# Kernel tuning notes

Hardware: AMD Instinct MI355X
Metric: run time of the kernel (lower is better)

The kernel has to match this reference:

```python
import jax, jax.numpy as jnp
import numpy as np

N_NODES = 100000
N_EDGES = 1600000
IN_DIM = 128
HIDDEN = 128
OUT_DIM = 10
N_GRAPHS = 512
N_LAYERS = 3


def setup_inputs() -> dict:
    key = jax.random.key(0)
    ks = jax.random.split(key, 12)
    s_in = 1.0 / np.sqrt(IN_DIM)
    s_h = 1.0 / np.sqrt(HIDDEN)
    return {
        "x": jax.random.normal(ks[0], (N_NODES, IN_DIM), jnp.float32),
        "lin1_w": jax.random.normal(ks[1], (IN_DIM, HIDDEN), jnp.float32) * s_in,
        "lin1_b": jnp.zeros((HIDDEN,), jnp.float32),
        "gcn_w": jax.random.normal(ks[2], (N_LAYERS, HIDDEN, HIDDEN), jnp.float32) * s_h,
        "gcn_b": jnp.zeros((N_LAYERS, HIDDEN), jnp.float32),
        "lin_out_w": jax.random.normal(ks[3], (HIDDEN, HIDDEN), jnp.float32) * s_h,
        "lin_out_b": jnp.zeros((HIDDEN,), jnp.float32),
        "cls_w": jax.random.normal(ks[4], (HIDDEN, OUT_DIM), jnp.float32) * s_h,
        "cls_b": jnp.zeros((OUT_DIM,), jnp.float32),
        "edge_index": jax.random.randint(ks[5], (2, N_EDGES), 0, N_NODES, jnp.int64),
        "batch": jnp.sort(jax.random.randint(ks[6], (N_NODES,), 0, N_GRAPHS, jnp.int64)),
    }


def reference(x, lin1_w, lin1_b, gcn_w, gcn_b, lin_out_w, lin_out_b, cls_w, cls_b, edge_index, batch):
    n = x.shape[0]
    # GCNConv normalization with added self-loops (PyG default)
    row, col = edge_index[0], edge_index[1]
    loop = jnp.arange(n)
    row2 = jnp.concatenate([row, loop])  # source (message origin)
    col2 = jnp.concatenate([col, loop])  # target (aggregation index)
    deg = jax.ops.segment_sum(jnp.ones_like(col2, dtype=x.dtype), col2, num_segments=n)
    dinv = jax.lax.rsqrt(jnp.maximum(deg, 1.0))
    norm = (dinv[row2] * dinv[col2])[:, None]  # [E+N, 1]

    counts = jax.ops.segment_sum(jnp.ones((n,), x.dtype), batch, num_segments=N_GRAPHS)
    counts = jnp.maximum(counts, 1.0)[:, None]

    def readout_mean(h):  # global_mean_pool -> [G, H]
        return jax.ops.segment_sum(h, batch, num_segments=N_GRAPHS) / counts

    # lin1 + elu (dropout = identity in eval mode)
    h = jax.nn.elu(x @ lin1_w + lin1_b)
    reps = readout_mean(h)  # readout_layers[0]; l_sum accumulates layer reps
    for i in range(N_LAYERS):
        hw = h @ gcn_w[i]                       # [N, H]
        msg = norm * hw[row2]                   # gather + scale
        agg = jax.ops.segment_sum(msg, col2, num_segments=n)  # scatter-add
        h = jax.nn.elu(agg + gcn_b[i])          # GCNConv bias then NaOp act
        # pooling op is 'none' (remove_pooling=True): graph unchanged
        reps = reps + readout_mean(h)           # readout_layers[i+1], summed by LaOp 'l_sum'
    g = jax.nn.elu(reps @ lin_out_w + lin_out_b)
    logits = g @ cls_w + cls_b
    return jax.nn.log_softmax(logits, axis=-1)
```

## Files before the change

### kernel.cpp

```cpp
#include <hip/hip_runtime.h>
#include <hip/hip_bf16.h>
#include <math.h>

#define NN 100000
#define NE 1600000
#define HID 128
#define NG 512
#define NB 512
#define RB 196
#define PCHUNK 4096
#define NPARTB ((NE + PCHUNK - 1) / PCHUNK)
#define GEMM_GRID ((NN + 127) / 128)

typedef unsigned short ushort_t;
typedef __attribute__((ext_vector_type(8))) short bf16x8;
typedef __attribute__((ext_vector_type(8))) unsigned short ushort8_t;
typedef __attribute__((ext_vector_type(4))) float f32x4;

__device__ __forceinline__ ushort_t f2bf(float v) {
    unsigned u = __float_as_uint(v);
    unsigned r = (u + 0x7FFF + ((u >> 16) & 1)) >> 16;
    return (ushort_t)r;
}
__device__ __forceinline__ float bf2f(ushort_t u) {
    return __uint_as_float((unsigned)u << 16);
}


__global__ __launch_bounds__(256) void hist_prepw(const int* __restrict__ ecol, int* __restrict__ bcount,
                                                  const float* __restrict__ lin1_w,
                                                  const float* __restrict__ gcn_w,
                                                  ushort_t* __restrict__ wt_hi,
                                                  ushort_t* __restrict__ wt_lo) {
    if (blockIdx.x < NPARTB) {
        __shared__ int lh[NB];
        const int blk = blockIdx.x, t = threadIdx.x;
        for (int i = t; i < NB; i += 256) lh[i] = 0;
        __syncthreads();
        const int e0 = blk * PCHUNK;
        const int e1 = min(e0 + PCHUNK, NE);
        for (int e = e0 + t; e < e1; e += 256) atomicAdd(&lh[ecol[e] / RB], 1);
        __syncthreads();
        for (int i = t; i < NB; i += 256) bcount[blk * NB + i] = lh[i];
    } else {
        int mb = blockIdx.x - NPARTB;
        int m = mb >> 3;
        int chunk = mb & 7;
        const float* W = (m == 0) ? lin1_w : gcn_w + (size_t)(m - 1) * 16384;
        ushort_t* hi = wt_hi + (size_t)m * 16384;
        ushort_t* lo = wt_lo + (size_t)m * 16384;
        for (int i = chunk * 2048 + threadIdx.x; i < (chunk + 1) * 2048; i += 256) {
            int j = i & 7;
            int lane = (i >> 3) & 63;
            int ks = (i >> 9) & 3;
            int ct = (i >> 11) & 7;
            int n = ct * 16 + (lane & 15);
            int k = ks * 32 + (lane >> 4) * 8 + j;
            float v = W[k * 128 + n];
            ushort_t h = f2bf(v);
            hi[i] = h;
            lo[i] = f2bf(v - bf2f(h));
        }
    }
}

__global__ __launch_bounds__(NB) void scan_bases(const int* __restrict__ bcount, int* __restrict__ basew,
                                                 int* __restrict__ brp, int* __restrict__ rp,
                                                 const int* __restrict__ batch, float* __restrict__ invcnt,
                                                 float* __restrict__ reps) {
    __shared__ int s[NB];
    int t = threadIdx.x;
    int tot = 0;
    for (int k = 0; k < NPARTB; ++k) {
        int c = bcount[k * NB + t];
        basew[k * NB + t] = tot;
        tot += c;
    }
    s[t] = tot;
    __syncthreads();
    for (int off = 1; off < NB; off <<= 1) {
        int x = (t >= off) ? s[t - off] : 0;
        __syncthreads();
        s[t] += x;
        __syncthreads();
    }
    int ex = s[t] - tot;
    brp[t] = ex;
    if (t == NB - 1) { brp[NB] = s[t]; rp[NN] = s[t]; }

    int lo = 0, hi = NN;
    while (lo < hi) { int m = (lo + hi) >> 1; if (batch[m] < t) lo = m + 1; else hi = m; }
    int s0 = lo;
    lo = 0; hi = NN;
    while (lo < hi) { int m = (lo + hi) >> 1; if (batch[m] < t + 1) lo = m + 1; else hi = m; }
    int c = lo - s0;
    invcnt[t] = 1.0f / (float)(c > 0 ? c : 1);

    f32x4 z = {0.f, 0.f, 0.f, 0.f};
    f32x4* rr = (f32x4*)(reps + (size_t)t * 128);
#pragma unroll
    for (int j = 0; j < 32; ++j) rr[j] = z;
}

template<int AMODE, int MODE>
__device__ __forceinline__ void gemm_body(int bid, int tid,
                                          const float* __restrict__ Af32,
                                          const ushort_t* __restrict__ a_bf,
                                          const ushort_t* __restrict__ wt_hi,
                                          const ushort_t* __restrict__ wt_lo,
                                          const float* __restrict__ bias,
                                          const float* __restrict__ dinv,
                                          ushort_t* __restrict__ out0,
                                          int N,
                                          ushort_t (* __restrict__ lt)[130]) {
    const int lane = tid & 63;
    const int wid = tid >> 6;
    const int rowBase = bid * 128 + wid * 32;
    const int rblk = rowBase >> 4;
    const int l15 = lane & 15, lg = lane >> 4;

    f32x4 acc[2][8];
#pragma unroll
    for (int rt = 0; rt < 2; ++rt)
#pragma unroll
        for (int ct = 0; ct < 8; ++ct) acc[rt][ct] = (f32x4){0.f, 0.f, 0.f, 0.f};

#pragma unroll
    for (int ks = 0; ks < 4; ++ks) {
        bf16x8 ahi[2], alo[2];
#pragma unroll
        for (int rt = 0; rt < 2; ++rt) {
            int r = rowBase + rt * 16 + l15;
            if (AMODE == 1) {
                float av[8];
                if (r < N) {
                    const float* ap = Af32 + (size_t)r * 128 + ks * 32 + lg * 8;
                    float4 a0 = *(const float4*)(ap);
                    float4 a1 = *(const float4*)(ap + 4);
                    av[0] = a0.x; av[1] = a0.y; av[2] = a0.z; av[3] = a0.w;
                    av[4] = a1.x; av[5] = a1.y; av[6] = a1.z; av[7] = a1.w;
                } else {
#pragma unroll
                    for (int j = 0; j < 8; ++j) av[j] = 0.f;
                }
#pragma unroll
                for (int j = 0; j < 8; ++j) {
                    ushort_t h = f2bf(av[j]);
                    ahi[rt][j] = (short)h;
                    alo[rt][j] = (short)f2bf(av[j] - bf2f(h));
                }
            } else {
                if (r < N) {
                    ahi[rt] = *(const bf16x8*)(a_bf + (size_t)(rblk + rt) * 2048 + (ks * 4 + lg) * 128 + l15 * 8);
                } else {
                    bf16x8 z = {0, 0, 0, 0, 0, 0, 0, 0};
                    ahi[rt] = z;
                }
            }
        }
#pragma unroll
        for (int ct = 0; ct < 8; ++ct) {
            size_t boff = (size_t)(((ct * 4 + ks) * 64 + lane) * 8);
            bf16x8 bhi = *(const bf16x8*)(wt_hi + boff);
            bf16x8 blo = *(const bf16x8*)(wt_lo + boff);
            acc[0][ct] = __builtin_amdgcn_mfma_f32_16x16x32_bf16(ahi[0], bhi, acc[0][ct], 0, 0, 0);
            acc[1][ct] = __builtin_amdgcn_mfma_f32_16x16x32_bf16(ahi[1], bhi, acc[1][ct], 0, 0, 0);
            acc[0][ct] = __builtin_amdgcn_mfma_f32_16x16x32_bf16(ahi[0], blo, acc[0][ct], 0, 0, 0);
            acc[1][ct] = __builtin_amdgcn_mfma_f32_16x16x32_bf16(ahi[1], blo, acc[1][ct], 0, 0, 0);
            if (AMODE == 1) {
                acc[0][ct] = __builtin_amdgcn_mfma_f32_16x16x32_bf16(alo[0], bhi, acc[0][ct], 0, 0, 0);
                acc[1][ct] = __builtin_amdgcn_mfma_f32_16x16x32_bf16(alo[1], bhi, acc[1][ct], 0, 0, 0);
            }
        }
    }

    if (MODE == 0) {
#pragma unroll
        for (int rt = 0; rt < 2; ++rt) {
#pragma unroll
            for (int reg = 0; reg < 4; ++reg) {
                int row = rowBase + rt * 16 + lg * 4 + reg;
                if (row >= N) continue;
                int r16 = lg * 4 + reg;
#pragma unroll
                for (int ct = 0; ct < 8; ++ct) {
                    int colc = ct * 16 + l15;
                    float v = acc[rt][ct][reg] + bias[colc];
                    v = v > 0.f ? v : expf(v) - 1.f;
                    out0[(size_t)(rblk + rt) * 2048 + (colc >> 3) * 128 + r16 * 8 + (colc & 7)] = f2bf(v);
                }
            }
        }
    } else {
#pragma unroll
        for (int rt = 0; rt < 2; ++rt) {
#pragma unroll
            for (int reg = 0; reg < 4; ++reg) {
                int row = rowBase + rt * 16 + lg * 4 + reg;
                if (row >= N) continue;
                float dv = dinv[row];
                int lr = rt * 16 + lg * 4 + reg;
#pragma unroll
                for (int ct = 0; ct < 8; ++ct) {
                    lt[lr][ct * 16 + l15] = f2bf(acc[rt][ct][reg] * dv);
                }
            }
        }
        __syncthreads();
#pragma unroll
        for (int it = 0; it < 8; ++it) {
            int idx = it * 64 + lane;
            int row = idx >> 4;
            int ch = idx & 15;
            int grow = rowBase + row;
            if (grow < N) {
                ushort8_t v8;
#pragma unroll
                for (int j = 0; j < 8; ++j) v8[j] = lt[row][ch * 8 + j];
                *(ushort8_t*)(out0 + (size_t)grow * 128 + ch * 8) = v8;
            }
        }
    }
}

__global__ __launch_bounds__(256) void part_gemm1(const int* __restrict__ erow, const int* __restrict__ ecol,
                                                  const int* __restrict__ brp, const int* __restrict__ basew,
                                                  unsigned int* __restrict__ pairs,
                                                  const float* __restrict__ x,
                                                  const ushort_t* __restrict__ wt_hi,
                                                  const ushort_t* __restrict__ wt_lo,
                                                  const float* __restrict__ lin1_b,
                                                  ushort_t* __restrict__ h) {
    if (blockIdx.x < NPARTB) {
        __shared__ int sbase[NB];
        __shared__ int lcnt[NB];
        const int blk = blockIdx.x, t = threadIdx.x;
        for (int i = t; i < NB; i += 256) {
            sbase[i] = brp[i] + basew[blk * NB + i];
            lcnt[i] = 0;
        }
        __syncthreads();
        const int e0 = blk * PCHUNK;
        const int e1 = min(e0 + PCHUNK, NE);
        for (int e = e0 + t; e < e1; e += 256) {
            int d = ecol[e];
            int b = d / RB;
            int off = atomicAdd(&lcnt[b], 1);
            pairs[sbase[b] + off] = ((unsigned)erow[e] << 8) | (unsigned)(d - b * RB);
        }
    } else {
        gemm_body<1, 0>(blockIdx.x - NPARTB, threadIdx.x, x, nullptr, wt_hi, wt_lo,
                        lin1_b, nullptr, h, NN, nullptr);
    }
}

__global__ __launch_bounds__(256) void fill_readout0(const unsigned int* __restrict__ pairs, const int* __restrict__ brp,
                                                     int* __restrict__ rp, float* __restrict__ dinv,
                                                     int* __restrict__ csrc,
                                                     const ushort_t* __restrict__ h,
                                                     const int* __restrict__ batch,
                                                     const float* __restrict__ invcnt,
                                                     float* __restrict__ reps) {
    if (blockIdx.x < NB) {
        __shared__ int cnt[RB];
        __shared__ int cur[RB];
        __shared__ int sc[256];
        const int b = blockIdx.x, t = threadIdx.x;
        const int nbase = b * RB;
        const int s = brp[b], e = brp[b + 1];
        for (int i = t; i < RB; i += 256) cnt[i] = 0;
        __syncthreads();
        for (int i = s + t; i < e; i += 256) atomicAdd(&cnt[pairs[i] & 255u], 1);
        __syncthreads();
        int v = (t < RB) ? cnt[t] : 0;
        sc[t] = v;
        __syncthreads();
        for (int off = 1; off < 256; off <<= 1) {
            int x = (t >= off) ? sc[t - off] : 0;
            __syncthreads();
            sc[t] += x;
            __syncthreads();
        }
        if (t < RB) {
            int ex = s + sc[t] - v;
            int node = nbase + t;
            if (node < NN) {
                rp[node] = ex;
                dinv[node] = rsqrtf((float)v + 1.0f);
            }
            cur[t] = ex;
        }
        __syncthreads();
        for (int i = s + t; i < e; i += 256) {
            unsigned int p = pairs[i];
            int slot = atomicAdd(&cur[p & 255u], 1);
            csrc[slot] = (int)(p >> 8);
        }
    } else {
        int bb = blockIdx.x - NB;
        int g = bb >> 2;
        int part = bb & 3;
        int lo = 0, hi = NN;
        while (lo < hi) { int m = (lo + hi) >> 1; if (batch[m] < g) lo = m + 1; else hi = m; }
        int s = lo;
        lo = 0; hi = NN;
        while (lo < hi) { int m = (lo + hi) >> 1; if (batch[m] < g + 1) lo = m + 1; else hi = m; }
        int e = lo;

        __shared__ float sh[16][136];
        int ns = (int)(threadIdx.x >> 4);
        int L  = (int)(threadIdx.x & 15);
        int c8 = L << 3;
        float acc[8] = {};
        for (int v = s + part + ns * 4; v < e; v += 64) {
            ushort8_t t = *(const ushort8_t*)(h + (size_t)(v >> 4) * 2048 + L * 128 + (v & 15) * 8);
#pragma unroll
            for (int j = 0; j < 8; ++j) acc[j] += bf2f(t[j]);
        }
#pragma unroll
        for (int j = 0; j < 8; ++j) sh[ns][c8 + j] = acc[j];
        __syncthreads();
        if (threadIdx.x < 128) {
            int c = (int)threadIdx.x;
            float sum = 0.f;
#pragma unroll
            for (int k = 0; k < 16; ++k) sum += sh[k][c];
            unsafeAtomicAdd(&reps[(size_t)g * 128 + c], sum * invcnt[g]);
        }
    }
}

__global__ __launch_bounds__(256) void gemm_gcn(const ushort_t* __restrict__ a_bf,
                                                const ushort_t* __restrict__ wt_hi,
                                                const ushort_t* __restrict__ wt_lo,
                                                const float* __restrict__ dinv,
                                                ushort_t* __restrict__ hwb) {
    __shared__ ushort_t lds[4][32][130];
    gemm_body<0, 1>(blockIdx.x, threadIdx.x, nullptr, a_bf, wt_hi, wt_lo,
                    nullptr, dinv, hwb, NN, lds[threadIdx.x >> 6]);
}

__global__ __launch_bounds__(256) void gather_agg(const int* __restrict__ rp,
                                                  const int* __restrict__ csrc,
                                                  const float* __restrict__ dinv,
                                                  const ushort_t* __restrict__ hwb,
                                                  const float* __restrict__ bias,
                                                  const int* __restrict__ batch,
                                                  const float* __restrict__ invcnt,
                                                  float* __restrict__ reps,
                                                  ushort_t* __restrict__ h_out) {
    __shared__ float sh[16][136];
    __shared__ int gid[16];
    const int v0 = blockIdx.x * 16;
    const int ns = (int)(threadIdx.x >> 4);
    int v = v0 + ns;
    int L = (int)(threadIdx.x & 15);
    int c8 = L << 3;
    if (threadIdx.x < 16) {
        int bidx = v0 + (int)threadIdx.x;
        if (bidx > NN - 1) bidx = NN - 1;
        gid[threadIdx.x] = batch[bidx];
    }

    float acc[8] = {};
    if (v < NN) {
        int s = rp[v], e = rp[v + 1];
        int i = s;
        for (; i + 16 <= e; i += 16) {
            int u[16];
#pragma unroll
            for (int k = 0; k < 16; ++k) u[k] = csrc[i + k];
            ushort8_t r[16];
#pragma unroll
            for (int k = 0; k < 16; ++k) r[k] = *(const ushort8_t*)(hwb + (size_t)u[k] * 128 + c8);
#pragma unroll
            for (int k = 0; k < 16; ++k)
#pragma unroll
                for (int j = 0; j < 8; ++j) acc[j] += bf2f(r[k][j]);
        }
        for (; i + 8 <= e; i += 8) {
            int u[8];
#pragma unroll
            for (int k = 0; k < 8; ++k) u[k] = csrc[i + k];
            ushort8_t r[8];
#pragma unroll
            for (int k = 0; k < 8; ++k) r[k] = *(const ushort8_t*)(hwb + (size_t)u[k] * 128 + c8);
#pragma unroll
            for (int k = 0; k < 8; ++k)
#pragma unroll
                for (int j = 0; j < 8; ++j) acc[j] += bf2f(r[k][j]);
        }
        for (; i < e; ++i) {
            int u = csrc[i];
            ushort8_t r0 = *(const ushort8_t*)(hwb + (size_t)u * 128 + c8);
#pragma unroll
            for (int j = 0; j < 8; ++j) acc[j] += bf2f(r0[j]);
        }

        float di = dinv[v];
        ushort8_t sv = *(const ushort8_t*)(hwb + (size_t)v * 128 + c8);
        ushort8_t o;
#pragma unroll
        for (int j = 0; j < 8; ++j) {
            float t = di * (acc[j] + bf2f(sv[j])) + bias[c8 + j];
            t = t > 0.f ? t : expf(t) - 1.f;
            acc[j] = t;
            o[j] = f2bf(t);
        }
        *(ushort8_t*)(h_out + (size_t)blockIdx.x * 2048 + L * 128 + ns * 8) = o;
    } else {
#pragma unroll
        for (int j = 0; j < 8; ++j) acc[j] = 0.f;
    }

#pragma unroll
    for (int j = 0; j < 8; ++j) sh[ns][c8 + j] = acc[j];
    __syncthreads();
    if (threadIdx.x < 128) {
        int c = (int)threadIdx.x;
        int nvalid = NN - v0;
        if (nvalid > 16) nvalid = 16;
        float run = sh[0][c];
        int cg = gid[0];
        for (int k = 1; k < nvalid; ++k) {
            int g2 = gid[k];
            if (g2 != cg) {
                unsafeAtomicAdd(&reps[(size_t)cg * 128 + c], run * invcnt[cg]);
                run = 0.f;
                cg = g2;
            }
            run += sh[k][c];
        }
        unsafeAtomicAdd(&reps[(size_t)cg * 128 + c], run * invcnt[cg]);
    }
}

__global__ __launch_bounds__(128) void head_fused(const float* __restrict__ reps,
                                                  const float* __restrict__ wout,
                                                  const float* __restrict__ bout,
                                                  const float* __restrict__ cw,
                                                  const float* __restrict__ cb,
                                                  float* __restrict__ out) {
    __shared__ float rrow[128];
    __shared__ float gg[128];
    __shared__ float lg[10];
    int t = threadIdx.x;
    int g = blockIdx.x;
    rrow[t] = reps[(size_t)g * 128 + t];
    __syncthreads();
    float a = bout[t];
    for (int k = 0; k < 128; ++k) a = fmaf(rrow[k], wout[k * 128 + t], a);
    a = a > 0.f ? a : expf(a) - 1.f;
    gg[t] = a;
    __syncthreads();
    if (t < 10) {
        float s = cb[t];
        for (int k = 0; k < 128; ++k) s = fmaf(gg[k], cw[k * 10 + t], s);
        lg[t] = s;
    }
    __syncthreads();
    if (t == 0) {
        float m = lg[0];
#pragma unroll
        for (int j = 1; j < 10; ++j) m = fmaxf(m, lg[j]);
        float se = 0.f;
#pragma unroll
        for (int j = 0; j < 10; ++j) se += expf(lg[j] - m);
        float L = logf(se);
#pragma unroll
        for (int j = 0; j < 10; ++j) out[(size_t)g * 10 + j] = lg[j] - m - L;
    }
}

extern "C" void kernel_launch(void* const* d_in, const int* in_sizes, int n_in,
                              void* d_out, int out_size, void* d_ws, size_t ws_size,
                              hipStream_t stream) {
    const float* x        = (const float*)d_in[0];
    const float* lin1_w   = (const float*)d_in[1];
    const float* lin1_b   = (const float*)d_in[2];
    const float* gcn_w    = (const float*)d_in[3];
    const float* gcn_b    = (const float*)d_in[4];
    const float* lin_out_w= (const float*)d_in[5];
    const float* lin_out_b= (const float*)d_in[6];
    const float* cls_w    = (const float*)d_in[7];
    const float* cls_b    = (const float*)d_in[8];
    const int*   ei       = (const int*)d_in[9];
    const int*   batch    = (const int*)d_in[10];
    float* out = (float*)d_out;

    const int* erow = ei;
    const int* ecol = ei + NE;

    ushort_t* h     = (ushort_t*)d_ws;
    ushort_t* hwb   = h + (size_t)NN * 128;
    float*    dinv  = (float*)(hwb + (size_t)NN * 128);
    float*    reps  = dinv + NN;
    float*    invcnt= reps + (size_t)NG * 128;
    int*      rp    = (int*)(invcnt + NG);
    int*      csrc  = rp + NN + 1;
    int*      brp   = csrc + NE;
    int*      bcount= brp + NB + 1;
    int*      basew = bcount + NPARTB * NB;
    ushort_t* wt_hi = (ushort_t*)(basew + NPARTB * NB);
    ushort_t* wt_lo = wt_hi + 4 * 16384;
    unsigned int* pairs = (unsigned int*)(wt_lo + 4 * 16384);

    hist_prepw<<<NPARTB + 32, 256, 0, stream>>>(ecol, bcount, lin1_w, gcn_w, wt_hi, wt_lo);
    scan_bases<<<1, NB, 0, stream>>>(bcount, basew, brp, rp, batch, invcnt, reps);
    part_gemm1<<<NPARTB + GEMM_GRID, 256, 0, stream>>>(erow, ecol, brp, basew, pairs,
                                                       x, wt_hi, wt_lo, lin1_b, h);
    fill_readout0<<<NB + NG * 4, 256, 0, stream>>>(pairs, brp, rp, dinv, csrc,
                                                   h, batch, invcnt, reps);

    for (int i = 0; i < 3; ++i) {
        gemm_gcn<<<GEMM_GRID, 256, 0, stream>>>(h, wt_hi + (size_t)(i + 1) * 16384,
                                                wt_lo + (size_t)(i + 1) * 16384,
                                                dinv, hwb);
        gather_agg<<<(NN + 15) / 16, 256, 0, stream>>>(rp, csrc, dinv, hwb,
                                                       gcn_b + (size_t)i * 128,
                                                       batch, invcnt, reps, h);
    }

    head_fused<<<NG, 128, 0, stream>>>(reps, lin_out_w, lin_out_b, cls_w, cls_b, out);
}
```

Measured before the change: 433.4 us.

## Stage edge partition and CSR fill in shared memory for coalesced writes

The partition kernel now counts edges per bucket, runs a local prefix scan, sorts the chunk's pairs into shared memory, then writes them out with contiguous global stores. Before, each edge was scattered straight to global memory at an atomic-assigned position. The CSR fill kernel likewise builds the per-bucket source list in shared memory and copies it out contiguously when the bucket fits under a cap, otherwise it falls back to direct scattering. This trades extra shared-memory traffic, barriers and more LDS per block (which may lower occupancy, including for the fused GEMM blocks) for more coalesced global writes.

Measured after the change: 435.7 us. About the same (+0.5%).

```diff
diff --git a/kernel.cpp b/kernel.cpp
--- a/kernel.cpp
+++ b/kernel.cpp
@@ -11,6 +11,7 @@
 #define PCHUNK 4096
 #define NPARTB ((NE + PCHUNK - 1) / PCHUNK)
 #define GEMM_GRID ((NN + 127) / 128)
+#define FILL_CAP 4352
 
 typedef unsigned short ushort_t;
 typedef __attribute__((ext_vector_type(8))) short bf16x8;
@@ -231,22 +232,51 @@
                                                   const ushort_t* __restrict__ wt_lo,
                                                   const float* __restrict__ lin1_b,
                                                   ushort_t* __restrict__ h) {
+    __shared__ unsigned smem[8448];
     if (blockIdx.x < NPARTB) {
-        __shared__ int sbase[NB];
-        __shared__ int lcnt[NB];
+        unsigned* spair = smem;
+        ushort_t* sbkt  = (ushort_t*)(smem + 4096);
+        int* cnt   = (int*)(smem + 6144);
+        int* lofs  = (int*)(smem + 6656);
+        int* cur   = (int*)(smem + 7168);
+        int* delta = (int*)(smem + 7680);
+        int* sc    = (int*)(smem + 8192);
+
         const int blk = blockIdx.x, t = threadIdx.x;
-        for (int i = t; i < NB; i += 256) {
-            sbase[i] = brp[i] + basew[blk * NB + i];
-            lcnt[i] = 0;
-        }
+        for (int i = t; i < NB; i += 256) cnt[i] = 0;
         __syncthreads();
         const int e0 = blk * PCHUNK;
         const int e1 = min(e0 + PCHUNK, NE);
+        for (int e = e0 + t; e < e1; e += 256) atomicAdd(&cnt[ecol[e] / RB], 1);
+        __syncthreads();
+        int c0 = cnt[2 * t], c1 = cnt[2 * t + 1];
+        sc[t] = c0 + c1;
+        __syncthreads();
+        for (int off = 1; off < 256; off <<= 1) {
+            int xv = (t >= off) ? sc[t - off] : 0;
+            __syncthreads();
+            sc[t] += xv;
+            __syncthreads();
+        }
+        int base2 = (t > 0) ? sc[t - 1] : 0;
+        lofs[2 * t] = base2;
+        lofs[2 * t + 1] = base2 + c0;
+        cur[2 * t] = base2;
+        cur[2 * t + 1] = base2 + c0;
+        delta[2 * t]     = brp[2 * t]     + basew[blk * NB + 2 * t]     - base2;
+        delta[2 * t + 1] = brp[2 * t + 1] + basew[blk * NB + 2 * t + 1] - (base2 + c0);
+        __syncthreads();
         for (int e = e0 + t; e < e1; e += 256) {
             int d = ecol[e];
             int b = d / RB;
-            int off = atomicAdd(&lcnt[b], 1);
-            pairs[sbase[b] + off] = ((unsigned)erow[e] << 8) | (unsigned)(d - b * RB);
+            int off = atomicAdd(&cur[b], 1);
+            spair[off] = ((unsigned)erow[e] << 8) | (unsigned)(d - b * RB);
+            sbkt[off] = (ushort_t)b;
+        }
+        __syncthreads();
+        const int nE = e1 - e0;
+        for (int i = t; i < nE; i += 256) {
+            pairs[delta[sbkt[i]] + i] = spair[i];
         }
     } else {
         gemm_body<1, 0>(blockIdx.x - NPARTB, threadIdx.x, x, nullptr, wt_hi, wt_lo,
@@ -261,13 +291,17 @@
                                                      const int* __restrict__ batch,
                                                      const float* __restrict__ invcnt,
                                                      float* __restrict__ reps) {
+    __shared__ unsigned smem[5120];
     if (blockIdx.x < NB) {
-        __shared__ int cnt[RB];
-        __shared__ int cur[RB];
-        __shared__ int sc[256];
+        int* scsr = (int*)smem;
+        int* cnt  = (int*)(smem + FILL_CAP);
+        int* cur  = (int*)(smem + FILL_CAP + 196);
+        int* sc   = (int*)(smem + FILL_CAP + 392);
+
         const int b = blockIdx.x, t = threadIdx.x;
         const int nbase = b * RB;
         const int s = brp[b], e = brp[b + 1];
+        const int Eb = e - s;
         for (int i = t; i < RB; i += 256) cnt[i] = 0;
         __syncthreads();
         for (int i = s + t; i < e; i += 256) atomicAdd(&cnt[pairs[i] & 255u], 1);
@@ -276,27 +310,39 @@
         sc[t] = v;
         __syncthreads();
         for (int off = 1; off < 256; off <<= 1) {
-            int x = (t >= off) ? sc[t - off] : 0;
+            int xv = (t >= off) ? sc[t - off] : 0;
             __syncthreads();
-            sc[t] += x;
+            sc[t] += xv;
             __syncthreads();
         }
         if (t < RB) {
-            int ex = s + sc[t] - v;
+            int lex = sc[t] - v;
             int node = nbase + t;
             if (node < NN) {
-                rp[node] = ex;
+                rp[node] = s + lex;
                 dinv[node] = rsqrtf((float)v + 1.0f);
             }
-            cur[t] = ex;
-        }
-        __syncthreads();
-        for (int i = s + t; i < e; i += 256) {
-            unsigned int p = pairs[i];
-            int slot = atomicAdd(&cur[p & 255u], 1);
-            csrc[slot] = (int)(p >> 8);
+            cur[t] = lex;
+        }
+        __syncthreads();
+        if (Eb <= FILL_CAP) {
+            for (int i = s + t; i < e; i += 256) {
+                unsigned int p = pairs[i];
+                int slot = atomicAdd(&cur[p & 255u], 1);
+                scsr[slot] = (int)(p >> 8);
+            }
+            __syncthreads();
+            for (int i = t; i < Eb; i += 256) csrc[s + i] = scsr[i];
+        } else {
+            for (int i = s + t; i < e; i += 256) {
+                unsigned int p = pairs[i];
+                int slot = atomicAdd(&cur[p & 255u], 1);
+                csrc[s + slot] = (int)(p >> 8);
+            }
         }
     } else {
+        float (*sh)[136] = (float (*)[136])smem;
+        int* gid = (int*)(smem + 16 * 136);
         int bb = blockIdx.x - NB;
         int g = bb >> 2;
         int part = bb & 3;
@@ -307,15 +353,14 @@
         while (lo < hi) { int m = (lo + hi) >> 1; if (batch[m] < g + 1) lo = m + 1; else hi = m; }
         int e = lo;
 
-        __shared__ float sh[16][136];
         int ns = (int)(threadIdx.x >> 4);
         int L  = (int)(threadIdx.x & 15);
         int c8 = L << 3;
         float acc[8] = {};
         for (int v = s + part + ns * 4; v < e; v += 64) {
-            ushort8_t t = *(const ushort8_t*)(h + (size_t)(v >> 4) * 2048 + L * 128 + (v & 15) * 8);
-#pragma unroll
-            for (int j = 0; j < 8; ++j) acc[j] += bf2f(t[j]);
+            ushort8_t t2 = *(const ushort8_t*)(h + (size_t)(v >> 4) * 2048 + L * 128 + (v & 15) * 8);
+#pragma unroll
+            for (int j = 0; j < 8; ++j) acc[j] += bf2f(t2[j]);
         }
 #pragma unroll
         for (int j = 0; j < 8; ++j) sh[ns][c8 + j] = acc[j];
```
